# Performance work log

Measured on AMD Instinct MI355X. Metric: run time of the kernel, lower is better.

The kernel has to match this reference:

```python
import jax, jax.numpy as jnp
import numpy as np

B, T, D, H = 32, 2048, 256, 256


def setup_inputs() -> dict:
    key = jax.random.key(0)
    k1, k2, k3, k4 = jax.random.split(key, 4)
    inputs = jax.random.normal(k1, (B, T, D), dtype=jnp.float32)
    lengths = jax.random.randint(k2, (B,), 0, T)
    # fused gate weights: order (i, f, g, o)
    Wi = jax.random.normal(k3, (D, 4 * H), dtype=jnp.float32) / np.sqrt(D)
    Wh = jax.random.normal(k4, (H, 4 * H), dtype=jnp.float32) / np.sqrt(H)
    b = jnp.zeros((4 * H,), dtype=jnp.float32)
    return {"inputs": inputs, "lengths": lengths, "Wi": Wi, "Wh": Wh, "b": b}


def reference(inputs, lengths, Wi, Wh, b):
    batch = inputs.shape[0]
    hid = Wh.shape[0]
    c0 = jnp.zeros((batch, hid), dtype=inputs.dtype)
    h0 = jnp.zeros((batch, hid), dtype=inputs.dtype)

    def step(carry, x_t):
        c, h = carry
        z = x_t @ Wi + h @ Wh + b  # [B, 4H]
        i, f, g, o = jnp.split(z, 4, axis=-1)
        new_c = jax.nn.sigmoid(f) * c + jax.nn.sigmoid(i) * jnp.tanh(g)
        new_h = jax.nn.sigmoid(o) * jnp.tanh(new_c)
        return (new_c, new_h), new_h

    xs = jnp.swapaxes(inputs, 0, 1)  # [T, B, D]
    _, hs = jax.lax.scan(step, (c0, h0), xs)  # hs: [T, B, H]
    idx = jnp.maximum(0, lengths - 1)
    return hs[idx, jnp.arange(batch), :]  # [B, H]
```

## Files before the change

kernel.cpp:

```cpp
#include <hip/hip_runtime.h>
#include <cstdint>
#include <cstddef>

#define NB 32
#define NT 2048
#define ND 256
#define NH 256
#define NG 1024
#define ROWS 16

#define TPB 512
#define KL  64
#define NQ  ((ND - KL) / 2)

typedef _Float16 h2_t __attribute__((ext_vector_type(2)));

__device__ __forceinline__ float sigf(float x) {
    return 1.0f / (1.0f + __expf(-x));
}
__device__ __forceinline__ float tanh_fast(float x) {
    return 2.0f / (1.0f + __expf(-2.0f * x)) - 1.0f;
}

__device__ __forceinline__ h2_t as_h2(uint32_t u) {
    union { uint32_t u; h2_t h; } c; c.u = u; return c.h;
}
__device__ __forceinline__ uint32_t packf16(float a, float b) {
    union { uint32_t u; h2_t h; } c;
    c.h[0] = (_Float16)a; c.h[1] = (_Float16)b;
    return c.u;
}
__device__ __forceinline__ float dot2(uint32_t hpack, uint32_t wpack, float acc) {
    return __builtin_amdgcn_fdot2(as_h2(hpack), as_h2(wpack), acc, false);
}

__global__ __launch_bounds__(256) void zx_kernel(const float* __restrict__ X,
                                                 const float* __restrict__ Wi,
                                                 const float* __restrict__ bias,
                                                 float* __restrict__ ZX) {
    __shared__ float xs[ROWS][ND];
    const int tid = threadIdx.x;
    const size_t row0 = (size_t)blockIdx.x * ROWS;

    const float4* Xv = (const float4*)(X + row0 * ND);
    float4* xsv = (float4*)(&xs[0][0]);
#pragma unroll
    for (int i = 0; i < (ROWS * ND / 4) / 256; ++i)
        xsv[tid + i * 256] = Xv[tid + i * 256];
    __syncthreads();

    const int j0 = tid * 4;
    const float4 bv = *(const float4*)(bias + j0);
    float acc[ROWS][4];
#pragma unroll
    for (int r = 0; r < ROWS; ++r) {
        acc[r][0] = bv.x; acc[r][1] = bv.y; acc[r][2] = bv.z; acc[r][3] = bv.w;
    }

    for (int k = 0; k < ND; ++k) {
        const float4 w = *(const float4*)(Wi + (size_t)k * NG + j0);
#pragma unroll
        for (int r = 0; r < ROWS; ++r) {
            const float x = xs[r][k];
            acc[r][0] = fmaf(x, w.x, acc[r][0]);
            acc[r][1] = fmaf(x, w.y, acc[r][1]);
            acc[r][2] = fmaf(x, w.z, acc[r][2]);
            acc[r][3] = fmaf(x, w.w, acc[r][3]);
        }
    }

#pragma unroll
    for (int r = 0; r < ROWS; ++r) {
        float4 o;
        o.x = acc[r][0]; o.y = acc[r][1]; o.z = acc[r][2]; o.w = acc[r][3];
        *(float4*)(ZX + (row0 + r) * NG + j0) = o;
    }
}

__global__
__attribute__((amdgpu_flat_work_group_size(TPB, TPB)))
__attribute__((amdgpu_waves_per_eu(2, 2)))
void rec_pers(const float* __restrict__ ZX,
              const float* __restrict__ Wh,
              const int* __restrict__ lengths,
              float* __restrict__ out)
{
    __shared__ uint4 lw[KL / 8][NG];
    __shared__ float zs[NG];
    __shared__ __align__(16) _Float16 hs_h[NH];

    const int b   = blockIdx.x;
    const int tid = threadIdx.x;
    const int j0  = tid;
    const int j1  = tid + 512;

#pragma unroll
    for (int r = 0; r < KL / 8; ++r) {
        const int k = 8 * r;
        uint4 p;
        p.x = packf16(Wh[(size_t)(k + 0) * NG + j0], Wh[(size_t)(k + 1) * NG + j0]);
        p.y = packf16(Wh[(size_t)(k + 2) * NG + j0], Wh[(size_t)(k + 3) * NG + j0]);
        p.z = packf16(Wh[(size_t)(k + 4) * NG + j0], Wh[(size_t)(k + 5) * NG + j0]);
        p.w = packf16(Wh[(size_t)(k + 6) * NG + j0], Wh[(size_t)(k + 7) * NG + j0]);
        lw[r][j0] = p;
        p.x = packf16(Wh[(size_t)(k + 0) * NG + j1], Wh[(size_t)(k + 1) * NG + j1]);
        p.y = packf16(Wh[(size_t)(k + 2) * NG + j1], Wh[(size_t)(k + 3) * NG + j1]);
        p.z = packf16(Wh[(size_t)(k + 4) * NG + j1], Wh[(size_t)(k + 5) * NG + j1]);
        p.w = packf16(Wh[(size_t)(k + 6) * NG + j1], Wh[(size_t)(k + 7) * NG + j1]);
        lw[r][j1] = p;
    }

    uint32_t wa[NQ], wb[NQ];
#pragma unroll
    for (int q = 0; q < NQ; ++q) {
        const int k = KL + 2 * q;
        uint32_t va = packf16(Wh[(size_t)k * NG + j0], Wh[(size_t)(k + 1) * NG + j0]);
        uint32_t vb = packf16(Wh[(size_t)k * NG + j1], Wh[(size_t)(k + 1) * NG + j1]);
        asm volatile("" : "+v"(va));
        asm volatile("" : "+v"(vb));
        wa[q] = va;
        wb[q] = vb;
    }

    if (tid < NH) hs_h[tid] = (_Float16)0.0f;
    float c = 0.0f, hlast = 0.0f;
    __syncthreads();

    const int len   = lengths[b];
    const int steps = (len < 1) ? 1 : len;

    for (int t = 0; t < steps; ++t) {
        const float zx0 = ZX[((size_t)b * NT + t) * NG + j0];
        const float zx1 = ZX[((size_t)b * NT + t) * NG + j1];

        float a0 = 0.0f, a1 = 0.0f;
        float b0 = 0.0f, b1 = 0.0f;

#pragma unroll
        for (int r = 0; r < KL / 8; ++r) {
            const uint4 h4 = *(const uint4*)(hs_h + 8 * r);
            const uint4 pa = lw[r][j0];
            const uint4 pb = lw[r][j1];
            a0 = dot2(h4.x, pa.x, a0); a1 = dot2(h4.y, pa.y, a1);
            a0 = dot2(h4.z, pa.z, a0); a1 = dot2(h4.w, pa.w, a1);
            b0 = dot2(h4.x, pb.x, b0); b1 = dot2(h4.y, pb.y, b1);
            b0 = dot2(h4.z, pb.z, b0); b1 = dot2(h4.w, pb.w, b1);
        }

#pragma unroll
        for (int m = 0; m < NQ / 4; ++m) {
            const uint4 h4 = *(const uint4*)(hs_h + KL + 8 * m);
            a0 = dot2(h4.x, wa[4 * m + 0], a0);
            a1 = dot2(h4.y, wa[4 * m + 1], a1);
            a0 = dot2(h4.z, wa[4 * m + 2], a0);
            a1 = dot2(h4.w, wa[4 * m + 3], a1);
            b0 = dot2(h4.x, wb[4 * m + 0], b0);
            b1 = dot2(h4.y, wb[4 * m + 1], b1);
            b0 = dot2(h4.z, wb[4 * m + 2], b0);
            b1 = dot2(h4.w, wb[4 * m + 3], b1);
        }

        zs[j0] = zx0 + a0 + a1;
        zs[j1] = zx1 + b0 + b1;
        __syncthreads();

        if (tid < NH) {
            const float iv = zs[tid];
            const float fv = zs[NH + tid];
            const float gv = zs[2 * NH + tid];
            const float ov = zs[3 * NH + tid];
            c = sigf(fv) * c + sigf(iv) * tanh_fast(gv);
            hlast = sigf(ov) * tanh_fast(c);
            hs_h[tid] = (_Float16)hlast;
        }
        __syncthreads();
    }

    if (tid < NH) out[(size_t)b * NH + tid] = hlast;
}

__global__ __launch_bounds__(512) void rec_fallback(
    const float* __restrict__ X,
    const float* __restrict__ Wi,
    const float* __restrict__ Wh,
    const float* __restrict__ bias,
    const int* __restrict__ lengths,
    float* __restrict__ out)
{
    __shared__ float hs[NH];
    __shared__ float zs[NG];
    __shared__ float xs[ND];

    const int b   = blockIdx.x;
    const int tid = threadIdx.x;
    const int c0  = tid * 2;

    const int len   = lengths[b];
    const int steps = (len < 1) ? 1 : len;

    float c_state = 0.0f;
    if (tid < NH) hs[tid] = 0.0f;
    const float b0 = bias[c0], b1 = bias[c0 + 1];
    __syncthreads();

    for (int t = 0; t < steps; ++t) {
        float a0 = b0, a1 = b1;
        if (tid < ND) xs[tid] = X[((size_t)b * NT + t) * ND + tid];
        __syncthreads();
#pragma unroll 2
        for (int k = 0; k < ND; k += 4) {
            const float4 xv = *(const float4*)(xs + k);
            const float2 w0 = *(const float2*)(Wi + (size_t)(k + 0) * NG + c0);
            const float2 w1 = *(const float2*)(Wi + (size_t)(k + 1) * NG + c0);
            const float2 w2 = *(const float2*)(Wi + (size_t)(k + 2) * NG + c0);
            const float2 w3 = *(const float2*)(Wi + (size_t)(k + 3) * NG + c0);
            a0 = fmaf(xv.x, w0.x, a0); a1 = fmaf(xv.x, w0.y, a1);
            a0 = fmaf(xv.y, w1.x, a0); a1 = fmaf(xv.y, w1.y, a1);
            a0 = fmaf(xv.z, w2.x, a0); a1 = fmaf(xv.z, w2.y, a1);
            a0 = fmaf(xv.w, w3.x, a0); a1 = fmaf(xv.w, w3.y, a1);
        }
#pragma unroll 2
        for (int k = 0; k < NH; k += 4) {
            const float4 hv = *(const float4*)(hs + k);
            const float2 w0 = *(const float2*)(Wh + (size_t)(k + 0) * NG + c0);
            const float2 w1 = *(const float2*)(Wh + (size_t)(k + 1) * NG + c0);
            const float2 w2 = *(const float2*)(Wh + (size_t)(k + 2) * NG + c0);
            const float2 w3 = *(const float2*)(Wh + (size_t)(k + 3) * NG + c0);
            a0 = fmaf(hv.x, w0.x, a0); a1 = fmaf(hv.x, w0.y, a1);
            a0 = fmaf(hv.y, w1.x, a0); a1 = fmaf(hv.y, w1.y, a1);
            a0 = fmaf(hv.z, w2.x, a0); a1 = fmaf(hv.z, w2.y, a1);
            a0 = fmaf(hv.w, w3.x, a0); a1 = fmaf(hv.w, w3.y, a1);
        }

        float2 zo2; zo2.x = a0; zo2.y = a1;
        *(float2*)(zs + c0) = zo2;
        __syncthreads();

        if (tid < NH) {
            const float iv = zs[tid];
            const float fv = zs[NH + tid];
            const float gv = zs[2 * NH + tid];
            const float ov = zs[3 * NH + tid];
            c_state = sigf(fv) * c_state + sigf(iv) * tanh_fast(gv);
            hs[tid] = sigf(ov) * tanh_fast(c_state);
        }
        __syncthreads();
    }

    if (tid < NH) out[(size_t)b * NH + tid] = hs[tid];
}

extern "C" void kernel_launch(void* const* d_in, const int* in_sizes, int n_in,
                              void* d_out, int out_size, void* d_ws, size_t ws_size,
                              hipStream_t stream) {
    const float* X       = (const float*)d_in[0];
    const int*   lengths = (const int*)d_in[1];
    const float* Wi      = (const float*)d_in[2];
    const float* Wh      = (const float*)d_in[3];
    const float* bias    = (const float*)d_in[4];
    float* out = (float*)d_out;

    const size_t zx_bytes = (size_t)NB * NT * NG * sizeof(float);
    float* ZX = (float*)d_ws;

    if (ws_size >= zx_bytes) {
        zx_kernel<<<dim3((NB * NT) / ROWS), dim3(256), 0, stream>>>(X, Wi, bias, ZX);
        rec_pers<<<dim3(NB), dim3(TPB), 0, stream>>>(ZX, Wh, lengths, out);
    } else {
        rec_fallback<<<dim3(NB), dim3(512), 0, stream>>>(X, Wi, Wh, bias, lengths, out);
    }
}
```

Measured before the change: 3.352 ms.

## Compute input projection with fp16 MFMA tiles instead of scalar FMA

Replaces the scalar fp32 input-projection GEMM with a 64x256-tile kernel that stages X in LDS as fp16 and uses 16x16x32 f16 MFMA instructions. Wi is converted to fp16 on the fly from global memory. The aim is to cut the time spent on the large precomputed X*Wi product ahead of the recurrence. This adds fp16 rounding of inputs and weights, which may affect accuracy, and uses strided global Wi reads and scalar output stores.

```diff
diff --git a/kernel.cpp b/kernel.cpp
--- a/kernel.cpp
+++ b/kernel.cpp
@@ -7,13 +7,14 @@
 #define ND 256
 #define NH 256
 #define NG 1024
-#define ROWS 16
 
 #define TPB 512
 #define KL  64
 #define NQ  ((ND - KL) / 2)
 
-typedef _Float16 h2_t __attribute__((ext_vector_type(2)));
+typedef _Float16 h2_t  __attribute__((ext_vector_type(2)));
+typedef _Float16 f16x8 __attribute__((ext_vector_type(8)));
+typedef float    f32x4 __attribute__((ext_vector_type(4)));
 
 __device__ __forceinline__ float sigf(float x) {
     return 1.0f / (1.0f + __expf(-x));
@@ -34,47 +35,71 @@
     return __builtin_amdgcn_fdot2(as_h2(hpack), as_h2(wpack), acc, false);
 }
 
-__global__ __launch_bounds__(256) void zx_kernel(const float* __restrict__ X,
-                                                 const float* __restrict__ Wi,
-                                                 const float* __restrict__ bias,
-                                                 float* __restrict__ ZX) {
-    __shared__ float xs[ROWS][ND];
-    const int tid = threadIdx.x;
-    const size_t row0 = (size_t)blockIdx.x * ROWS;
+__global__ __launch_bounds__(256) void zx_mfma(const float* __restrict__ X,
+                                               const float* __restrict__ Wi,
+                                               const float* __restrict__ bias,
+                                               float* __restrict__ ZX)
+{
+    __shared__ _Float16 XL[64][264];
+
+    const int t    = threadIdx.x;
+    const int mblk = blockIdx.x;
+    const int nblk = blockIdx.y;
+    const size_t row0 = (size_t)mblk * 64;
+    const int n0   = nblk * 256;
+    const int l    = t & 63;
+    const int w    = t >> 6;
+    const int cc   = l & 15;
+    const int g    = l >> 4;
+    const int wm   = (w & 1) * 32;
+    const int wn   = (w >> 1) * 128;
 
     const float4* Xv = (const float4*)(X + row0 * ND);
-    float4* xsv = (float4*)(&xs[0][0]);
-#pragma unroll
-    for (int i = 0; i < (ROWS * ND / 4) / 256; ++i)
-        xsv[tid + i * 256] = Xv[tid + i * 256];
+#pragma unroll
+    for (int i = 0; i < 16; ++i) {
+        const int q   = i * 256 + t;
+        const int row = q >> 6;
+        const int c4  = q & 63;
+        const float4 v = Xv[q];
+        _Float16* dst = &XL[row][c4 * 4];
+        dst[0] = (_Float16)v.x; dst[1] = (_Float16)v.y;
+        dst[2] = (_Float16)v.z; dst[3] = (_Float16)v.w;
+    }
     __syncthreads();
 
-    const int j0 = tid * 4;
-    const float4 bv = *(const float4*)(bias + j0);
-    float acc[ROWS][4];
-#pragma unroll
-    for (int r = 0; r < ROWS; ++r) {
-        acc[r][0] = bv.x; acc[r][1] = bv.y; acc[r][2] = bv.z; acc[r][3] = bv.w;
-    }
-
-    for (int k = 0; k < ND; ++k) {
-        const float4 w = *(const float4*)(Wi + (size_t)k * NG + j0);
-#pragma unroll
-        for (int r = 0; r < ROWS; ++r) {
-            const float x = xs[r][k];
-            acc[r][0] = fmaf(x, w.x, acc[r][0]);
-            acc[r][1] = fmaf(x, w.y, acc[r][1]);
-            acc[r][2] = fmaf(x, w.z, acc[r][2]);
-            acc[r][3] = fmaf(x, w.w, acc[r][3]);
-        }
-    }
-
-#pragma unroll
-    for (int r = 0; r < ROWS; ++r) {
-        float4 o;
-        o.x = acc[r][0]; o.y = acc[r][1]; o.z = acc[r][2]; o.w = acc[r][3];
-        *(float4*)(ZX + (row0 + r) * NG + j0) = o;
-    }
+    f32x4 acc[2][8];
+#pragma unroll
+    for (int nt = 0; nt < 8; ++nt) {
+        const float bv = bias[n0 + wn + nt * 16 + cc];
+        f32x4 a; a[0] = bv; a[1] = bv; a[2] = bv; a[3] = bv;
+        acc[0][nt] = a; acc[1][nt] = a;
+    }
+
+#pragma unroll
+    for (int kt = 0; kt < 8; ++kt) {
+        const f16x8 av0 = *(const f16x8*)&XL[wm +      cc][kt * 32 + 8 * g];
+        const f16x8 av1 = *(const f16x8*)&XL[wm + 16 + cc][kt * 32 + 8 * g];
+#pragma unroll
+        for (int nt = 0; nt < 8; ++nt) {
+            const float* wp = Wi + (size_t)(kt * 32 + 8 * g) * NG
+                              + n0 + wn + nt * 16 + cc;
+            f16x8 bv;
+#pragma unroll
+            for (int j = 0; j < 8; ++j) bv[j] = (_Float16)wp[(size_t)j * NG];
+            acc[0][nt] = __builtin_amdgcn_mfma_f32_16x16x32_f16(av0, bv, acc[0][nt], 0, 0, 0);
+            acc[1][nt] = __builtin_amdgcn_mfma_f32_16x16x32_f16(av1, bv, acc[1][nt], 0, 0, 0);
+        }
+    }
+
+#pragma unroll
+    for (int m = 0; m < 2; ++m)
+#pragma unroll
+        for (int nt = 0; nt < 8; ++nt)
+#pragma unroll
+            for (int r = 0; r < 4; ++r) {
+                const size_t row = row0 + wm + 16 * m + 4 * g + r;
+                ZX[row * NG + n0 + wn + nt * 16 + cc] = acc[m][nt][r];
+            }
 }
 
 __global__
@@ -264,7 +289,7 @@
     float* ZX = (float*)d_ws;
 
     if (ws_size >= zx_bytes) {
-        zx_kernel<<<dim3((NB * NT) / ROWS), dim3(256), 0, stream>>>(X, Wi, bias, ZX);
+        zx_mfma<<<dim3((NB * NT) / 64, NG / 256), dim3(256), 0, stream>>>(X, Wi, bias, ZX);
         rec_pers<<<dim3(NB), dim3(TPB), 0, stream>>>(ZX, Wh, lengths, out);
     } else {
         rec_fallback<<<dim3(NB), dim3(512), 0, stream>>>(X, Wi, Wh, bias, lengths, out);
```

Result: faster. 3.129 ms, median of 2 (-6.6%).
